# Kernel tuning notes

Measured on AMD Instinct MI355X. Metric: run time of the kernel, lower is better.

## Reference

```python
import jax, jax.numpy as jnp
import numpy as np

# config (matches init_kwargs)
B, N, C_IN = 2, 16384, 64
NPOINT, NSAMPLE, RADIUS = 2048, 32, 0.8
MLP = [64, 128, 256]
EPS = 1e-5


def _fps(xyz, npoint):
    """Furthest point sampling. xyz: (B,N,3) -> idx (B,npoint) int32."""
    b, n, _ = xyz.shape
    d0 = jnp.sum((xyz - xyz[:, :1, :]) ** 2, -1)  # dist to point 0

    def body(mind, _):
        nxt = jnp.argmax(mind, -1)                       # (B,)
        pt = jnp.take_along_axis(xyz, nxt[:, None, None], 1)  # (B,1,3)
        mind = jnp.minimum(mind, jnp.sum((xyz - pt) ** 2, -1))
        return mind, nxt

    _, idxs = jax.lax.scan(body, d0, None, length=npoint - 1)  # (npoint-1,B)
    idxs = jnp.concatenate([jnp.zeros((1, b), idxs.dtype), idxs], 0)
    return jnp.transpose(idxs).astype(jnp.int32)


def _ball_query(xyz, new_xyz, radius, nsample):
    """First nsample neighbors within radius (pointnet2 semantics: pad with first hit)."""
    n = xyz.shape[1]
    d = jnp.sum((new_xyz[:, :, None, :] - xyz[:, None, :, :]) ** 2, -1)  # (B,np,N)
    mask = d < radius * radius
    # prefer lowest original index among in-range points
    score = jnp.where(mask, -jnp.arange(n, dtype=jnp.float32), -(n + 1.0))
    vals, idxs = jax.lax.top_k(score, nsample)           # (B,np,ns)
    valid = vals > -(n + 0.5)
    idx = jnp.where(valid, idxs, idxs[..., :1])
    cnt = mask.sum(-1)                                    # (B,np)
    return idx.astype(jnp.int32), cnt


def _gather(arr, idx):  # arr (B,N,...), idx (B,...) -> (B,...,...)
    return jax.vmap(lambda a, i: a[i])(arr, idx)


def _bn_eval4(x, g, b):  # (B,C,P,S), eval-mode BN with running mean 0 / var 1
    s = g / jnp.sqrt(1.0 + EPS)
    return x * s[None, :, None, None] + b[None, :, None, None]


def _bn_eval3(x, g, b):  # (B,C,S)
    s = g / jnp.sqrt(1.0 + EPS)
    return x * s[None, :, None] + b[None, :, None]


def setup_inputs() -> dict:
    key = jax.random.key(0)
    ks = jax.random.split(key, 12)
    xyz = jax.random.normal(ks[0], (B, N, 3), jnp.float32)
    features = jax.random.normal(ks[1], (B, C_IN, N), jnp.float32)
    cin = 3 + C_IN
    dims = [cin] + MLP
    inp = {"xyz": xyz, "features": features}
    for li in range(3):
        w = jax.random.normal(ks[2 + li], (dims[li + 1], dims[li]), jnp.float32) / np.sqrt(dims[li])
        inp[f"W{li+1}"] = w
        inp[f"g{li+1}"] = jnp.ones((dims[li + 1],), jnp.float32)
        inp[f"b{li+1}"] = jnp.zeros((dims[li + 1],), jnp.float32)
    npt8, cd, cd8 = NPOINT // 8, MLP[-1], MLP[-1] // 8
    inp["Wq"] = jax.random.normal(ks[5], (npt8, NPOINT), jnp.float32) / np.sqrt(NPOINT)
    inp["gq"] = jnp.ones((npt8,), jnp.float32)
    inp["bq"] = jnp.zeros((npt8,), jnp.float32)
    inp["Wk"] = jax.random.normal(ks[6], (npt8, NPOINT), jnp.float32) / np.sqrt(NPOINT)
    inp["gk"] = jnp.ones((npt8,), jnp.float32)
    inp["bk"] = jnp.zeros((npt8,), jnp.float32)
    inp["We1"] = jax.random.normal(ks[7], (cd8, cd), jnp.float32) / np.sqrt(cd)
    inp["We2"] = jax.random.normal(ks[8], (cd, cd8), jnp.float32) / np.sqrt(cd8)
    inp["alpha"] = jnp.zeros((1,), jnp.float32)  # torch: nn.Parameter(torch.zeros(1))
    return inp


def reference(xyz, features, W1, g1, b1, W2, g2, b2, W3, g3, b3,
              Wq, gq, bq, Wk, gk, bk, We1, We2, alpha):
    # ---- d-FPS sampling (indices are non-differentiable, as in the CUDA op) ----
    xyz_c = jax.lax.stop_gradient(xyz)
    samp = _fps(xyz_c, NPOINT)                       # (B,np)
    new_xyz = _gather(xyz, samp)                     # (B,np,3)
    # ---- ball query + grouping ----
    nn_idx, cnt = _ball_query(xyz_c, jax.lax.stop_gradient(new_xyz), RADIUS, NSAMPLE)
    grouped_xyz = _gather(xyz, nn_idx) - new_xyz[:, :, None, :]        # (B,np,ns,3)
    grouped_feat = _gather(jnp.transpose(features, (0, 2, 1)), nn_idx)  # (B,np,ns,C)
    h = jnp.transpose(jnp.concatenate([grouped_xyz, grouped_feat], -1), (0, 3, 1, 2))  # (B,3+C,np,ns)
    # ---- shared MLP (1x1 conv + BN(eval) + ReLU) ----
    for (w, g, b) in ((W1, g1, b1), (W2, g2, b2), (W3, g3, b3)):
        h = jax.nn.relu(_bn_eval4(jnp.einsum('oi,bips->bops', w, h), g, b))
    h = h * (cnt > 0)[:, None, :, None].astype(h.dtype)  # mask empty balls
    x = jnp.max(h, axis=-1)                               # (B,Cd,np) max-pool over nsample
    # ---- LCEF channel-affinity attention ----
    xh = jnp.transpose(x, (0, 2, 1))                      # (B,np,Cd)
    q = jax.nn.relu(_bn_eval3(jnp.einsum('oi,bis->bos', Wq, xh), gq, bq))  # (B,np/8,Cd)
    k = jax.nn.relu(_bn_eval3(jnp.einsum('oi,bis->bos', Wk, xh), gk, bk))  # (B,np/8,Cd)
    sim = jnp.einsum('bqc,bqd->bcd', k, q)                # (B,Cd,Cd)
    aff = jax.nn.softmax(jnp.max(sim, -1, keepdims=True) - sim, axis=-1)
    s = jnp.max(x, -1)                                    # (B,Cd) squeeze
    e = jax.nn.sigmoid(jnp.einsum('oi,bi->bo', We2, jax.nn.relu(jnp.einsum('oi,bi->bo', We1, s))))
    v = x * e[:, :, None]                                 # excitation
    out = alpha[0] * jnp.einsum('bcd,bdn->bcn', aff, v) + x
    return new_xyz, out
```

## Files before the change

kernel.cpp:

```cpp
#include <hip/hip_runtime.h>
#include <hip/hip_bf16.h>

typedef unsigned short ushort_t;
typedef unsigned int uint_t;
typedef unsigned long long ull_t;
typedef float v2f __attribute__((ext_vector_type(2)));

#define B_    2
#define N_    16384
#define NP_   2048
#define NS_   32
#define EPSF  1e-5f

__device__ __forceinline__ float bf2f(ushort_t u) { return __uint_as_float(((uint_t)u) << 16); }

__device__ __forceinline__ float dist2(float dx, float dy, float dz) {
  return __fadd_rn(__fadd_rn(__fmul_rn(dx, dx), __fmul_rn(dy, dy)), __fmul_rn(dz, dz));
}

template<int CTRL, int RMASK>
__device__ __forceinline__ float dppmax(float x) {
  int m = __builtin_amdgcn_update_dpp(0, __float_as_int(x), CTRL, RMASK, 0xf, true);
  return fmaxf(x, __int_as_float(m));
}
__device__ __forceinline__ float rlanef(float x, int l) {
  return __int_as_float(__builtin_amdgcn_readlane(__float_as_int(x), l));
}

__global__ void k_flag(const uint_t* __restrict__ g1w, int* __restrict__ flag) {
  if (threadIdx.x == 0 && blockIdx.x == 0)
    flag[0] = (g1w[0] == 0x3F803F80u) ? 1 : 0;
}

struct CvtTab { const void* src[18]; };
__constant__ int c_psz[18] = {4288, 64, 64, 8192, 128, 128, 32768, 256, 256,
                              524288, 256, 256, 524288, 256, 256, 8192, 8192, 1};
__constant__ int c_poff[18] = {0, 4288, 4352, 4416, 12608, 12736, 12864, 45632, 45888,
                               46144, 570432, 570688, 570944, 1095232, 1095488,
                               1095744, 1103936, 1112128};

__global__ void k_cvt_all(CvtTab tab, float* __restrict__ par, const int* __restrict__ flagp) {
  int p = blockIdx.y;
  int n = c_psz[p];
  int i = blockIdx.x * 256 + threadIdx.x;
  if (i >= n) return;
  float v = flagp[0] ? bf2f(((const ushort_t*)tab.src[p])[i]) : ((const float*)tab.src[p])[i];
  par[c_poff[p] + i] = v;
}

__global__ void k_wt(const float* __restrict__ W1f, const float* __restrict__ W2f,
                     const float* __restrict__ W3f, float* __restrict__ Wt) {
  int which = blockIdx.y;
  int i = blockIdx.x * 256 + threadIdx.x;
  if (which == 0) {
    if (i >= 4288) return;
    int o = i / 67, k = i - o * 67;
    Wt[k * 64 + o] = W1f[i];
  } else if (which == 1) {
    if (i >= 8192) return;
    int o = i >> 6, k = i & 63;
    Wt[4288 + k * 128 + o] = W2f[i];
  } else {
    if (i >= 32768) return;
    int o = i >> 7, k = i & 127;
    Wt[12480 + k * 256 + o] = W3f[i];
  }
}

__global__ void k_xyz_soa(const void* __restrict__ xyz, const int* __restrict__ flagp,
                          float* __restrict__ X, float* __restrict__ Y, float* __restrict__ Z) {
  int g = blockIdx.x * blockDim.x + threadIdx.x;
  if (g >= B_ * N_) return;
  if (flagp[0]) {
    const ushort_t* p = (const ushort_t*)xyz;
    X[g] = bf2f(p[g * 3 + 0]); Y[g] = bf2f(p[g * 3 + 1]); Z[g] = bf2f(p[g * 3 + 2]);
  } else {
    const float* p = (const float*)xyz;
    X[g] = p[g * 3 + 0]; Y[g] = p[g * 3 + 1]; Z[g] = p[g * 3 + 2];
  }
}

__global__ void k_featT(const void* __restrict__ feat, const int* __restrict__ flagp,
                        float* __restrict__ featF) {
  __shared__ float tile[64 * 65];
  int b = blockIdx.x >> 8, n0 = (blockIdx.x & 255) * 64, t = threadIdx.x;
  int f = flagp[0];
  for (int i = t; i < 4096; i += 256) {
    int c = i >> 6, nn = i & 63;
    size_t src = (size_t)(b * 64 + c) * N_ + n0 + nn;
    tile[c * 65 + nn] = f ? bf2f(((const ushort_t*)feat)[src]) : ((const float*)feat)[src];
  }
  __syncthreads();
  for (int i = t; i < 4096; i += 256) {
    int nn = i >> 6, c = i & 63;
    featF[((size_t)(b * N_ + n0 + nn)) * 64 + c] = tile[c * 65 + nn];
  }
}

__global__ __launch_bounds__(1024)
__attribute__((amdgpu_waves_per_eu(4, 4)))
void k_fps13(const float* __restrict__ X,
             const float* __restrict__ Y,
             const float* __restrict__ Z,
             float* __restrict__ nxf,
             void* __restrict__ outp,
             const int* __restrict__ flagp) {
  __shared__ float sv[16];
  __shared__ float bc[4];
  int b = blockIdx.x, t = threadIdx.x;
  int lane = t & 63, wid = t >> 6;
  int f = flagp[0];
  const float* Xb = X + b * N_;
  const float* Yb = Y + b * N_;
  const float* Zb = Z + b * N_;
  float cx = Xb[0], cy = Yb[0], cz = Zb[0];
  if (t == 0) {
    int base = b * NP_ * 3;
    nxf[base + 0] = cx; nxf[base + 1] = cy; nxf[base + 2] = cz;
    if (f) {
      __hip_bfloat16* o = (__hip_bfloat16*)outp;
      o[base + 0] = __float2bfloat16(cx); o[base + 1] = __float2bfloat16(cy); o[base + 2] = __float2bfloat16(cz);
    } else {
      float* o = (float*)outp;
      o[base + 0] = cx; o[base + 1] = cy; o[base + 2] = cz;
    }
  }
  v2f xv[8], yv[8], zv[8], mdv[8];
  {
#pragma clang fp contract(off)
    v2f cx2 = (v2f){cx, cx}, cy2 = (v2f){cy, cy}, cz2 = (v2f){cz, cz};
#pragma unroll
    for (int c = 0; c < 4; c++) {
      float4 xq = ((const float4*)Xb)[(t << 2) + c];
      float4 yq = ((const float4*)Yb)[(t << 2) + c];
      float4 zq = ((const float4*)Zb)[(t << 2) + c];
      xv[2 * c + 0] = (v2f){xq.x, xq.y}; xv[2 * c + 1] = (v2f){xq.z, xq.w};
      yv[2 * c + 0] = (v2f){yq.x, yq.y}; yv[2 * c + 1] = (v2f){yq.z, yq.w};
      zv[2 * c + 0] = (v2f){zq.x, zq.y}; zv[2 * c + 1] = (v2f){zq.z, zq.w};
#pragma unroll
      for (int h = 0; h < 2; h++) {
        int i = 2 * c + h;
        v2f dx = xv[i] - cx2;
        v2f dy = yv[i] - cy2;
        v2f dz = zv[i] - cz2;
        mdv[i] = dx * dx + dy * dy + dz * dz;
      }
    }
  }
#pragma unroll
  for (int k = 0; k < 8; k++)
    asm volatile("" : "+v"(xv[k]), "+v"(yv[k]), "+v"(zv[k]));

  for (int it = 1; it < NP_; it++) {
    float a0 = fmaxf(fmaxf(mdv[0].x, mdv[0].y), fmaxf(mdv[1].x, mdv[1].y));
    float a1 = fmaxf(fmaxf(mdv[2].x, mdv[2].y), fmaxf(mdv[3].x, mdv[3].y));
    float a2 = fmaxf(fmaxf(mdv[4].x, mdv[4].y), fmaxf(mdv[5].x, mdv[5].y));
    float a3 = fmaxf(fmaxf(mdv[6].x, mdv[6].y), fmaxf(mdv[7].x, mdv[7].y));
    float lm = fmaxf(fmaxf(a0, a1), fmaxf(a2, a3));
    float v = lm;
    v = dppmax<0x111, 0xf>(v);
    v = dppmax<0x112, 0xf>(v);
    v = dppmax<0x114, 0xf>(v);
    v = dppmax<0x118, 0xf>(v);
    v = dppmax<0x142, 0xa>(v);
    v = dppmax<0x143, 0xc>(v);
    float wm = rlanef(v, 63);
    ull_t m1 = __ballot(lm == wm);
    int wlead = __ffsll((unsigned long long)m1) - 1;
    if (lane == wlead) sv[wid] = wm;
    __syncthreads();
    float pv = sv[lane & 15];
    float q = pv;
    q = dppmax<0x111, 0xf>(q);
    q = dppmax<0x112, 0xf>(q);
    q = dppmax<0x114, 0xf>(q);
    q = dppmax<0x118, 0xf>(q);
    float bm = rlanef(q, 15);
    ull_t m2 = __ballot((lane < 16) && (pv == bm));
    int wwave = __ffsll((unsigned long long)m2) - 1;
    if (wid == wwave && lane == wlead) {
      float wx = xv[0].x, wy = yv[0].x, wz = zv[0].x;
#pragma unroll
      for (int k = 15; k >= 0; k--) {
        float mk = (k & 1) ? mdv[k >> 1].y : mdv[k >> 1].x;
        if (mk == lm) {
          wx = (k & 1) ? xv[k >> 1].y : xv[k >> 1].x;
          wy = (k & 1) ? yv[k >> 1].y : yv[k >> 1].x;
          wz = (k & 1) ? zv[k >> 1].y : zv[k >> 1].x;
        }
      }
      bc[0] = wx; bc[1] = wy; bc[2] = wz;
      int base = (b * NP_ + it) * 3;
      nxf[base + 0] = wx; nxf[base + 1] = wy; nxf[base + 2] = wz;
      if (f) {
        __hip_bfloat16* o = (__hip_bfloat16*)outp;
        o[base + 0] = __float2bfloat16(wx); o[base + 1] = __float2bfloat16(wy); o[base + 2] = __float2bfloat16(wz);
      } else {
        float* o = (float*)outp;
        o[base + 0] = wx; o[base + 1] = wy; o[base + 2] = wz;
      }
    }
    __syncthreads();
    cx = bc[0]; cy = bc[1]; cz = bc[2];
    {
#pragma clang fp contract(off)
      v2f cx2 = (v2f){cx, cx}, cy2 = (v2f){cy, cy}, cz2 = (v2f){cz, cz};
#pragma unroll
      for (int k = 0; k < 8; k++) {
        v2f dx = xv[k] - cx2;
        v2f dy = yv[k] - cy2;
        v2f dz = zv[k] - cz2;
        v2f d = dx * dx + dy * dy + dz * dz;
        mdv[k] = __builtin_elementwise_min(mdv[k], d);
      }
    }
  }
}

__global__ void k_ball(const float* __restrict__ X, const float* __restrict__ Y,
                       const float* __restrict__ Z, const float* __restrict__ nxf,
                       int* __restrict__ nnidx) {
  __shared__ int ibuf[4][NS_];
  int t = threadIdx.x, w = t >> 6, lane = t & 63;
  int cid = blockIdx.x * 4 + w;
  int b = cid >> 11;
  const float* Xb = X + b * N_;
  const float* Yb = Y + b * N_;
  const float* Zb = Z + b * N_;
  float cx = nxf[cid * 3 + 0], cy = nxf[cid * 3 + 1], cz = nxf[cid * 3 + 2];
  int found = 0;
  for (int c = 0; c < N_ / 64; c++) {
    int n = c * 64 + lane;
    float d = dist2(Xb[n] - cx, Yb[n] - cy, Zb[n] - cz);
    bool pred = d < 0.64f;
    ull_t mask = __ballot(pred);
    if (pred) {
      int rank = found + __popcll(mask & ((1ull << lane) - 1ull));
      if (rank < NS_) ibuf[w][rank] = n;
    }
    found += __popcll(mask);
    if (found >= NS_) break;
  }
  __syncthreads();
  if (lane < NS_) {
    int idx = (lane < found) ? ibuf[w][lane] : ibuf[w][0];
    nnidx[cid * NS_ + lane] = idx;
  }
}

__global__ __launch_bounds__(256) void k_mlp(
    const float* __restrict__ featF, const float* __restrict__ X,
    const float* __restrict__ Y, const float* __restrict__ Z,
    const float* __restrict__ nxf, const int* __restrict__ nnidx,
    const float* __restrict__ Wt,
    const float* __restrict__ g1f, const float* __restrict__ b1f,
    const float* __restrict__ g2f, const float* __restrict__ b2f,
    const float* __restrict__ g3f, const float* __restrict__ b3f,
    float* __restrict__ x_nc) {
  __shared__ __align__(16) char smem[33280];
  float* h2f = (float*)smem;
  float* h0f = (float*)(smem + 16384);
  float* h1f = (float*)(smem + 24960);
  int* idxs  = (int*)(smem + 33152);
  const float* Wt1 = Wt;
  const float* Wt2 = Wt + 4288;
  const float* Wt3 = Wt + 12480;

  int t = threadIdx.x;
  int cid = blockIdx.x;
  int b = cid >> 11;
  if (t < 32) idxs[t] = nnidx[cid * NS_ + t];
  __syncthreads();
  float cx = nxf[cid * 3 + 0], cy = nxf[cid * 3 + 1], cz = nxf[cid * 3 + 2];
  if (t < 32) {
    int n = b * N_ + idxs[t];
    h0f[0 * 32 + t] = X[n] - cx;
    h0f[1 * 32 + t] = Y[n] - cy;
    h0f[2 * 32 + t] = Z[n] - cz;
  }
  {
    int s = t >> 3, cg = t & 7;
    const float* fr = featF + ((size_t)(b * N_ + idxs[s])) * 64 + cg * 8;
    float4 a = ((const float4*)fr)[0];
    float4 c2 = ((const float4*)fr)[1];
    int kb = 3 + cg * 8;
    h0f[(kb + 0) * 32 + s] = a.x;  h0f[(kb + 1) * 32 + s] = a.y;
    h0f[(kb + 2) * 32 + s] = a.z;  h0f[(kb + 3) * 32 + s] = a.w;
    h0f[(kb + 4) * 32 + s] = c2.x; h0f[(kb + 5) * 32 + s] = c2.y;
    h0f[(kb + 6) * 32 + s] = c2.z; h0f[(kb + 7) * 32 + s] = c2.w;
  }
  __syncthreads();

  int og = t >> 3, sg = t & 7;
  int s0 = sg * 4;
  {
    int o0 = og * 2;
    float acc[2][4] = {{0, 0, 0, 0}, {0, 0, 0, 0}};
    for (int k = 0; k < 67; k++) {
      float4 h = *(const float4*)(h0f + k * 32 + s0);
      float2 wp = *(const float2*)(Wt1 + k * 64 + o0);
      acc[0][0] = fmaf(wp.x, h.x, acc[0][0]);
      acc[0][1] = fmaf(wp.x, h.y, acc[0][1]);
      acc[0][2] = fmaf(wp.x, h.z, acc[0][2]);
      acc[0][3] = fmaf(wp.x, h.w, acc[0][3]);
      acc[1][0] = fmaf(wp.y, h.x, acc[1][0]);
      acc[1][1] = fmaf(wp.y, h.y, acc[1][1]);
      acc[1][2] = fmaf(wp.y, h.z, acc[1][2]);
      acc[1][3] = fmaf(wp.y, h.w, acc[1][3]);
    }
#pragma unroll
    for (int i2 = 0; i2 < 2; i2++) {
      int o = o0 + i2;
      float sc = g1f[o] / sqrtf(1.0f + EPSF);
      float bb = b1f[o];
      float4 yv;
      yv.x = fmaxf(fmaf(acc[i2][0], sc, bb), 0.0f);
      yv.y = fmaxf(fmaf(acc[i2][1], sc, bb), 0.0f);
      yv.z = fmaxf(fmaf(acc[i2][2], sc, bb), 0.0f);
      yv.w = fmaxf(fmaf(acc[i2][3], sc, bb), 0.0f);
      *(float4*)(h1f + o * 32 + s0) = yv;
    }
  }
  __syncthreads();
  {
    int o0 = og * 4;
    float acc[4][4] = {{0,0,0,0},{0,0,0,0},{0,0,0,0},{0,0,0,0}};
    for (int k = 0; k < 64; k++) {
      float4 h = *(const float4*)(h1f + k * 32 + s0);
      float4 wp = *(const float4*)(Wt2 + k * 128 + o0);
      float w[4] = {wp.x, wp.y, wp.z, wp.w};
#pragma unroll
      for (int i2 = 0; i2 < 4; i2++) {
        acc[i2][0] = fmaf(w[i2], h.x, acc[i2][0]);
        acc[i2][1] = fmaf(w[i2], h.y, acc[i2][1]);
        acc[i2][2] = fmaf(w[i2], h.z, acc[i2][2]);
        acc[i2][3] = fmaf(w[i2], h.w, acc[i2][3]);
      }
    }
#pragma unroll
    for (int i2 = 0; i2 < 4; i2++) {
      int o = o0 + i2;
      float sc = g2f[o] / sqrtf(1.0f + EPSF);
      float bb = b2f[o];
      float4 yv;
      yv.x = fmaxf(fmaf(acc[i2][0], sc, bb), 0.0f);
      yv.y = fmaxf(fmaf(acc[i2][1], sc, bb), 0.0f);
      yv.z = fmaxf(fmaf(acc[i2][2], sc, bb), 0.0f);
      yv.w = fmaxf(fmaf(acc[i2][3], sc, bb), 0.0f);
      *(float4*)(h2f + o * 32 + s0) = yv;
    }
  }
  __syncthreads();
  float acc3[8][4] = {{0,0,0,0},{0,0,0,0},{0,0,0,0},{0,0,0,0},
                      {0,0,0,0},{0,0,0,0},{0,0,0,0},{0,0,0,0}};
  int o0 = og * 8;
  for (int kg = 0; kg < 128; kg++) {
    float4 h = *(const float4*)(h2f + kg * 32 + s0);
    float4 wa = *(const float4*)(Wt3 + kg * 256 + o0);
    float4 wc = *(const float4*)(Wt3 + kg * 256 + o0 + 4);
    float w[8] = {wa.x, wa.y, wa.z, wa.w, wc.x, wc.y, wc.z, wc.w};
#pragma unroll
    for (int i2 = 0; i2 < 8; i2++) {
      acc3[i2][0] = fmaf(w[i2], h.x, acc3[i2][0]);
      acc3[i2][1] = fmaf(w[i2], h.y, acc3[i2][1]);
      acc3[i2][2] = fmaf(w[i2], h.z, acc3[i2][2]);
      acc3[i2][3] = fmaf(w[i2], h.w, acc3[i2][3]);
    }
  }
  float mx[8];
#pragma unroll
  for (int i2 = 0; i2 < 8; i2++) {
    int o = o0 + i2;
    float sc = g3f[o] / sqrtf(1.0f + EPSF);
    float bb = b3f[o];
    float m0 = fmaxf(fmaf(acc3[i2][0], sc, bb), 0.0f);
    float m1 = fmaxf(fmaf(acc3[i2][1], sc, bb), 0.0f);
    float m2 = fmaxf(fmaf(acc3[i2][2], sc, bb), 0.0f);
    float m3 = fmaxf(fmaf(acc3[i2][3], sc, bb), 0.0f);
    mx[i2] = fmaxf(fmaxf(m0, m1), fmaxf(m2, m3));
  }
#pragma unroll
  for (int off = 1; off < 8; off <<= 1) {
#pragma unroll
    for (int i2 = 0; i2 < 8; i2++) mx[i2] = fmaxf(mx[i2], __shfl_xor(mx[i2], off));
  }
  if (sg == 0) {
    float4 a, c;
    a.x = mx[0]; a.y = mx[1]; a.z = mx[2]; a.w = mx[3];
    c.x = mx[4]; c.y = mx[5]; c.z = mx[6]; c.w = mx[7];
    *(float4*)(x_nc + (size_t)cid * 256 + o0) = a;
    *(float4*)(x_nc + (size_t)cid * 256 + o0 + 4) = c;
  }
}

__global__ __launch_bounds__(256) void k_sqe(const float* __restrict__ x_nc,
                                             const float* __restrict__ We1f,
                                             const float* __restrict__ We2f,
                                             float* __restrict__ e) {
  __shared__ float ssh[256];
  __shared__ float ush[32];
  int b = blockIdx.x, t = threadIdx.x;
  const float* xb = x_nc + (size_t)b * NP_ * 256;
  float m = -1e30f;
#pragma unroll 8
  for (int n = 0; n < NP_; n++) m = fmaxf(m, xb[(size_t)n * 256 + t]);
  ssh[t] = m;
  __syncthreads();
  if (t < 32) {
    float a = 0.0f;
    for (int i = 0; i < 256; i++) a = fmaf(We1f[t * 256 + i], ssh[i], a);
    ush[t] = fmaxf(a, 0.0f);
  }
  __syncthreads();
  float a = 0.0f;
#pragma unroll
  for (int j = 0; j < 32; j++) a = fmaf(We2f[t * 32 + j], ush[j], a);
  e[b * 256 + t] = 1.0f / (1.0f + expf(-a));
}

__global__ __launch_bounds__(256) void k_qk(const float* __restrict__ x_nc,
                                            const float* __restrict__ Wqf, const float* __restrict__ gqf, const float* __restrict__ bqf,
                                            const float* __restrict__ Wkf, const float* __restrict__ gkf, const float* __restrict__ bkf,
                                            float* __restrict__ qb, float* __restrict__ kb) {
  __shared__ float As[64 * 33];
  __shared__ float Bs[32 * 64];
  int bid = blockIdx.x;
  int b = bid & 1, tq = (bid >> 1) & 1, mt = (bid >> 2) & 3, nt = (bid >> 4) & 3;
  const float* W = tq ? Wkf : Wqf;
  const float* g = tq ? gkf : gqf;
  const float* bb_ = tq ? bkf : bqf;
  float* outp = tq ? kb : qb;
  int t = threadIdx.x;
  int o0 = (t >> 4) * 4, c0 = (t & 15) * 4;
  float acc[4][4] = {{0,0,0,0},{0,0,0,0},{0,0,0,0},{0,0,0,0}};
  for (int k0 = 0; k0 < NP_; k0 += 32) {
    for (int i = t; i < 2048; i += 256) {
      int row = i >> 5, kk = i & 31;
      As[row * 33 + kk] = W[(size_t)(mt * 64 + row) * NP_ + k0 + kk];
    }
    for (int i = t; i < 2048; i += 256) {
      int kk = i >> 6, cc = i & 63;
      Bs[kk * 64 + cc] = x_nc[((size_t)(b * NP_ + k0 + kk)) * 256 + nt * 64 + cc];
    }
    __syncthreads();
    for (int kk = 0; kk < 32; kk++) {
      float4 bv = *(const float4*)(Bs + kk * 64 + c0);
      float a0 = As[(o0 + 0) * 33 + kk];
      float a1 = As[(o0 + 1) * 33 + kk];
      float a2 = As[(o0 + 2) * 33 + kk];
      float a3 = As[(o0 + 3) * 33 + kk];
      acc[0][0] = fmaf(a0, bv.x, acc[0][0]); acc[0][1] = fmaf(a0, bv.y, acc[0][1]);
      acc[0][2] = fmaf(a0, bv.z, acc[0][2]); acc[0][3] = fmaf(a0, bv.w, acc[0][3]);
      acc[1][0] = fmaf(a1, bv.x, acc[1][0]); acc[1][1] = fmaf(a1, bv.y, acc[1][1]);
      acc[1][2] = fmaf(a1, bv.z, acc[1][2]); acc[1][3] = fmaf(a1, bv.w, acc[1][3]);
      acc[2][0] = fmaf(a2, bv.x, acc[2][0]); acc[2][1] = fmaf(a2, bv.y, acc[2][1]);
      acc[2][2] = fmaf(a2, bv.z, acc[2][2]); acc[2][3] = fmaf(a2, bv.w, acc[2][3]);
      acc[3][0] = fmaf(a3, bv.x, acc[3][0]); acc[3][1] = fmaf(a3, bv.y, acc[3][1]);
      acc[3][2] = fmaf(a3, bv.z, acc[3][2]); acc[3][3] = fmaf(a3, bv.w, acc[3][3]);
    }
    __syncthreads();
  }
#pragma unroll
  for (int i2 = 0; i2 < 4; i2++) {
    int o = mt * 64 + o0 + i2;
    float sc = g[o] / sqrtf(1.0f + EPSF);
    float bv = bb_[o];
    float4 y;
    y.x = fmaxf(fmaf(acc[i2][0], sc, bv), 0.0f);
    y.y = fmaxf(fmaf(acc[i2][1], sc, bv), 0.0f);
    y.z = fmaxf(fmaf(acc[i2][2], sc, bv), 0.0f);
    y.w = fmaxf(fmaf(acc[i2][3], sc, bv), 0.0f);
    *(float4*)(outp + ((size_t)(b * 256 + o)) * 256 + nt * 64 + c0) = y;
  }
}

__global__ __launch_bounds__(256) void k_sim(const float* __restrict__ qb,
                                             const float* __restrict__ kb,
                                             float* __restrict__ sim) {
  __shared__ float As[32 * 64];
  __shared__ float Bs[32 * 64];
  int bid = blockIdx.x;
  int b = bid & 1, ct = (bid >> 1) & 3, dt = (bid >> 3) & 3;
  int t = threadIdx.x;
  int c0 = (t >> 4) * 4, d0 = (t & 15) * 4;
  float acc[4][4] = {{0,0,0,0},{0,0,0,0},{0,0,0,0},{0,0,0,0}};
  for (int k0 = 0; k0 < 256; k0 += 32) {
    for (int i = t; i < 2048; i += 256) {
      int kk = i >> 6, cc = i & 63;
      As[kk * 64 + cc] = kb[((size_t)(b * 256 + k0 + kk)) * 256 + ct * 64 + cc];
      Bs[kk * 64 + cc] = qb[((size_t)(b * 256 + k0 + kk)) * 256 + dt * 64 + cc];
    }
    __syncthreads();
    for (int kk = 0; kk < 32; kk++) {
      float4 av = *(const float4*)(As + kk * 64 + c0);
      float4 bv = *(const float4*)(Bs + kk * 64 + d0);
      acc[0][0] = fmaf(av.x, bv.x, acc[0][0]); acc[0][1] = fmaf(av.x, bv.y, acc[0][1]);
      acc[0][2] = fmaf(av.x, bv.z, acc[0][2]); acc[0][3] = fmaf(av.x, bv.w, acc[0][3]);
      acc[1][0] = fmaf(av.y, bv.x, acc[1][0]); acc[1][1] = fmaf(av.y, bv.y, acc[1][1]);
      acc[1][2] = fmaf(av.y, bv.z, acc[1][2]); acc[1][3] = fmaf(av.y, bv.w, acc[1][3]);
      acc[2][0] = fmaf(av.z, bv.x, acc[2][0]); acc[2][1] = fmaf(av.z, bv.y, acc[2][1]);
      acc[2][2] = fmaf(av.z, bv.z, acc[2][2]); acc[2][3] = fmaf(av.z, bv.w, acc[2][3]);
      acc[3][0] = fmaf(av.w, bv.x, acc[3][0]); acc[3][1] = fmaf(av.w, bv.y, acc[3][1]);
      acc[3][2] = fmaf(av.w, bv.z, acc[3][2]); acc[3][3] = fmaf(av.w, bv.w, acc[3][3]);
    }
    __syncthreads();
  }
#pragma unroll
  for (int i2 = 0; i2 < 4; i2++) {
    *(float4*)(sim + ((size_t)(b * 256 + ct * 64 + c0 + i2)) * 256 + dt * 64 + d0) =
        *(float4*)acc[i2];
  }
}

__global__ void k_aff(const float* __restrict__ sim, float* __restrict__ aff) {
  int t = threadIdx.x, w = t >> 6, lane = t & 63;
  int row = blockIdx.x * 4 + w;
  const float* sr = sim + (size_t)row * 256;
  float4 v = *(const float4*)(sr + lane * 4);
  float mx = fmaxf(fmaxf(v.x, v.y), fmaxf(v.z, v.w));
#pragma unroll
  for (int off = 32; off >= 1; off >>= 1) mx = fmaxf(mx, __shfl_xor(mx, off));
  float4 u;
  u.x = mx - v.x; u.y = mx - v.y; u.z = mx - v.z; u.w = mx - v.w;
  float um = fmaxf(fmaxf(u.x, u.y), fmaxf(u.z, u.w));
#pragma unroll
  for (int off = 32; off >= 1; off >>= 1) um = fmaxf(um, __shfl_xor(um, off));
  float4 p;
  p.x = expf(u.x - um); p.y = expf(u.y - um); p.z = expf(u.z - um); p.w = expf(u.w - um);
  float s = ((p.x + p.y) + (p.z + p.w));
#pragma unroll
  for (int off = 32; off >= 1; off >>= 1) s += __shfl_xor(s, off);
  float4 o;
  o.x = p.x / s; o.y = p.y / s; o.z = p.z / s; o.w = p.w / s;
  *(float4*)(aff + (size_t)row * 256 + lane * 4) = o;
}

__global__ __launch_bounds__(256) void k_out(const float* __restrict__ aff,
                                             const float* __restrict__ x_nc,
                                             const float* __restrict__ e,
                                             const float* __restrict__ alphaf,
                                             void* __restrict__ outp,
                                             const int* __restrict__ flagp) {
  __shared__ float Acs[64 * 33];
  __shared__ float Bs[32 * 65];
  __shared__ float Xs[64 * 65];
  int bid = blockIdx.x;
  int b = bid & 1, ct = (bid >> 1) & 3, nt = bid >> 3;
  int t = threadIdx.x;
  int c0 = (t >> 4) * 4, n0 = (t & 15) * 4;
  float acc[4][4] = {{0,0,0,0},{0,0,0,0},{0,0,0,0},{0,0,0,0}};
  for (int k0 = 0; k0 < 256; k0 += 32) {
    for (int i = t; i < 2048; i += 256) {
      int cc = i >> 5, kk = i & 31;
      Acs[cc * 33 + kk] = aff[((size_t)(b * 256 + ct * 64 + cc)) * 256 + k0 + kk];
    }
    for (int i = t; i < 2048; i += 256) {
      int nn = i >> 5, kk = i & 31;
      Bs[kk * 65 + nn] =
          x_nc[((size_t)(b * NP_ + nt * 64 + nn)) * 256 + k0 + kk] * e[b * 256 + k0 + kk];
    }
    __syncthreads();
    for (int kk = 0; kk < 32; kk++) {
      float a0 = Acs[(c0 + 0) * 33 + kk];
      float a1 = Acs[(c0 + 1) * 33 + kk];
      float a2 = Acs[(c0 + 2) * 33 + kk];
      float a3 = Acs[(c0 + 3) * 33 + kk];
      float b0 = Bs[kk * 65 + n0 + 0];
      float b1 = Bs[kk * 65 + n0 + 1];
      float b2 = Bs[kk * 65 + n0 + 2];
      float b3 = Bs[kk * 65 + n0 + 3];
      acc[0][0] = fmaf(a0, b0, acc[0][0]); acc[0][1] = fmaf(a0, b1, acc[0][1]);
      acc[0][2] = fmaf(a0, b2, acc[0][2]); acc[0][3] = fmaf(a0, b3, acc[0][3]);
      acc[1][0] = fmaf(a1, b0, acc[1][0]); acc[1][1] = fmaf(a1, b1, acc[1][1]);
      acc[1][2] = fmaf(a1, b2, acc[1][2]); acc[1][3] = fmaf(a1, b3, acc[1][3]);
      acc[2][0] = fmaf(a2, b0, acc[2][0]); acc[2][1] = fmaf(a2, b1, acc[2][1]);
      acc[2][2] = fmaf(a2, b2, acc[2][2]); acc[2][3] = fmaf(a2, b3, acc[2][3]);
      acc[3][0] = fmaf(a3, b0, acc[3][0]); acc[3][1] = fmaf(a3, b1, acc[3][1]);
      acc[3][2] = fmaf(a3, b2, acc[3][2]); acc[3][3] = fmaf(a3, b3, acc[3][3]);
    }
    __syncthreads();
  }
  for (int i = t; i < 4096; i += 256) {
    int nn = i >> 6, cc = i & 63;
    Xs[nn * 65 + cc] = x_nc[((size_t)(b * NP_ + nt * 64 + nn)) * 256 + ct * 64 + cc];
  }
  __syncthreads();
  float af = alphaf[0];
  int f = flagp[0];
#pragma unroll
  for (int i2 = 0; i2 < 4; i2++) {
    int c = ct * 64 + c0 + i2;
#pragma unroll
    for (int j = 0; j < 4; j++) {
      float xv = Xs[(n0 + j) * 65 + (c0 + i2)];
      float y = af * acc[i2][j] + xv;
      size_t base = 12288 + ((size_t)(b * 256 + c)) * NP_ + nt * 64 + n0 + j;
      if (f) ((__hip_bfloat16*)outp)[base] = __float2bfloat16(y);
      else   ((float*)outp)[base] = y;
    }
  }
}

extern "C" void kernel_launch(void* const* d_in, const int* in_sizes, int n_in,
                              void* d_out, int out_size, void* d_ws, size_t ws_size,
                              hipStream_t stream) {
  char* ws = (char*)d_ws;
  int*   flag  = (int*)(ws + 0);
  float* X     = (float*)(ws + 64);
  float* Y     = (float*)(ws + 131136);
  float* Z     = (float*)(ws + 262208);
  float* featF = (float*)(ws + 393280);
  float* par   = (float*)(ws + 8781888);
  float* nxf   = (float*)(ws + 13230464);
  int*   nn    = (int*)(ws + 13279616);
  float* x_nc  = (float*)(ws + 13803904);
  float* qb    = (float*)(ws + 17998208);
  float* kb    = (float*)(ws + 18522496);
  float* sim   = (float*)(ws + 19046784);
  float* aff   = (float*)(ws + 19571072);
  float* evec  = (float*)(ws + 20095360);
  float* Wt    = qb;

  float* W1f = par + 0,      *g1f = par + 4288,    *b1f = par + 4352;
  float* W2f = par + 4416,   *g2f = par + 12608,   *b2f = par + 12736;
  float* W3f = par + 12864,  *g3f = par + 45632,   *b3f = par + 45888;
  float* Wqf = par + 46144,  *gqf = par + 570432,  *bqf = par + 570688;
  float* Wkf = par + 570944, *gkf = par + 1095232, *bkf = par + 1095488;
  float* We1f = par + 1095744, *We2f = par + 1103936, *alphaf = par + 1112128;

  k_flag<<<dim3(1), dim3(64), 0, stream>>>((const uint_t*)d_in[3], flag);

  CvtTab tab;
  for (int p = 0; p < 18; p++) tab.src[p] = d_in[2 + p];
  k_cvt_all<<<dim3(2048, 18), dim3(256), 0, stream>>>(tab, par, flag);
  k_wt<<<dim3(128, 3), dim3(256), 0, stream>>>(W1f, W2f, W3f, Wt);

  k_xyz_soa<<<dim3(128), dim3(256), 0, stream>>>(d_in[0], flag, X, Y, Z);
  k_featT<<<dim3(512), dim3(256), 0, stream>>>(d_in[1], flag, featF);
  k_fps13<<<dim3(2), dim3(1024), 0, stream>>>(X, Y, Z, nxf, d_out, flag);
  k_ball<<<dim3(1024), dim3(256), 0, stream>>>(X, Y, Z, nxf, nn);
  k_mlp<<<dim3(4096), dim3(256), 0, stream>>>(featF, X, Y, Z, nxf, nn, Wt,
                                              g1f, b1f, g2f, b2f, g3f, b3f, x_nc);
  k_sqe<<<dim3(2), dim3(256), 0, stream>>>(x_nc, We1f, We2f, evec);
  k_qk<<<dim3(64), dim3(256), 0, stream>>>(x_nc, Wqf, gqf, bqf, Wkf, gkf, bkf, qb, kb);
  k_sim<<<dim3(32), dim3(256), 0, stream>>>(qb, kb, sim);
  k_aff<<<dim3(128), dim3(256), 0, stream>>>(sim, aff);
  k_out<<<dim3(256), dim3(256), 0, stream>>>(aff, x_nc, evec, alphaf, d_out, flag);
}
```

Baseline: 4.094 ms.

## Remove second per-iteration barrier in FPS via double-buffered per-wave candidates

Each wave leader now finds its own candidate point coordinates and writes value plus xyz into a double-buffered shared array. After the single barrier, every thread picks the winning wave's coordinates directly, so the second __syncthreads and the broadcast slot are gone. The local max reduction also uses packed v2f max operations. Every wave leader now does the 16-way coordinate selection, adding a little redundant work and shared memory to halve the barrier count per iteration.

```diff
diff --git a/kernel.cpp b/kernel.cpp
--- a/kernel.cpp
+++ b/kernel.cpp
@@ -99,14 +99,16 @@
 
 __global__ __launch_bounds__(1024)
 __attribute__((amdgpu_waves_per_eu(4, 4)))
-void k_fps13(const float* __restrict__ X,
+void k_fps14(const float* __restrict__ X,
              const float* __restrict__ Y,
              const float* __restrict__ Z,
              float* __restrict__ nxf,
              void* __restrict__ outp,
              const int* __restrict__ flagp) {
-  __shared__ float sv[16];
-  __shared__ float bc[4];
+  __shared__ float sv[2][16];
+  __shared__ float sx[2][16];
+  __shared__ float sy[2][16];
+  __shared__ float sz[2][16];
   int b = blockIdx.x, t = threadIdx.x;
   int lane = t & 63, wid = t >> 6;
   int f = flagp[0];
@@ -152,11 +154,15 @@
     asm volatile("" : "+v"(xv[k]), "+v"(yv[k]), "+v"(zv[k]));
 
   for (int it = 1; it < NP_; it++) {
-    float a0 = fmaxf(fmaxf(mdv[0].x, mdv[0].y), fmaxf(mdv[1].x, mdv[1].y));
-    float a1 = fmaxf(fmaxf(mdv[2].x, mdv[2].y), fmaxf(mdv[3].x, mdv[3].y));
-    float a2 = fmaxf(fmaxf(mdv[4].x, mdv[4].y), fmaxf(mdv[5].x, mdv[5].y));
-    float a3 = fmaxf(fmaxf(mdv[6].x, mdv[6].y), fmaxf(mdv[7].x, mdv[7].y));
-    float lm = fmaxf(fmaxf(a0, a1), fmaxf(a2, a3));
+    int buf = it & 1;
+    v2f m01 = __builtin_elementwise_max(mdv[0], mdv[1]);
+    v2f m23 = __builtin_elementwise_max(mdv[2], mdv[3]);
+    v2f m45 = __builtin_elementwise_max(mdv[4], mdv[5]);
+    v2f m67 = __builtin_elementwise_max(mdv[6], mdv[7]);
+    v2f m03 = __builtin_elementwise_max(m01, m23);
+    v2f m47 = __builtin_elementwise_max(m45, m67);
+    v2f m07 = __builtin_elementwise_max(m03, m47);
+    float lm = fmaxf(m07.x, m07.y);
     float v = lm;
     v = dppmax<0x111, 0xf>(v);
     v = dppmax<0x112, 0xf>(v);
@@ -167,9 +173,24 @@
     float wm = rlanef(v, 63);
     ull_t m1 = __ballot(lm == wm);
     int wlead = __ffsll((unsigned long long)m1) - 1;
-    if (lane == wlead) sv[wid] = wm;
+    if (lane == wlead) {
+      float wx = xv[0].x, wy = yv[0].x, wz = zv[0].x;
+#pragma unroll
+      for (int k = 15; k >= 0; k--) {
+        float mk = (k & 1) ? mdv[k >> 1].y : mdv[k >> 1].x;
+        if (mk == lm) {
+          wx = (k & 1) ? xv[k >> 1].y : xv[k >> 1].x;
+          wy = (k & 1) ? yv[k >> 1].y : yv[k >> 1].x;
+          wz = (k & 1) ? zv[k >> 1].y : zv[k >> 1].x;
+        }
+      }
+      sv[buf][wid] = lm;
+      sx[buf][wid] = wx;
+      sy[buf][wid] = wy;
+      sz[buf][wid] = wz;
+    }
     __syncthreads();
-    float pv = sv[lane & 15];
+    float pv = sv[buf][lane & 15];
     float q = pv;
     q = dppmax<0x111, 0xf>(q);
     q = dppmax<0x112, 0xf>(q);
@@ -178,30 +199,20 @@
     float bm = rlanef(q, 15);
     ull_t m2 = __ballot((lane < 16) && (pv == bm));
     int wwave = __ffsll((unsigned long long)m2) - 1;
-    if (wid == wwave && lane == wlead) {
-      float wx = xv[0].x, wy = yv[0].x, wz = zv[0].x;
-#pragma unroll
-      for (int k = 15; k >= 0; k--) {
-        float mk = (k & 1) ? mdv[k >> 1].y : mdv[k >> 1].x;
-        if (mk == lm) {
-          wx = (k & 1) ? xv[k >> 1].y : xv[k >> 1].x;
-          wy = (k & 1) ? yv[k >> 1].y : yv[k >> 1].x;
-          wz = (k & 1) ? zv[k >> 1].y : zv[k >> 1].x;
-        }
-      }
-      bc[0] = wx; bc[1] = wy; bc[2] = wz;
+    cx = sx[buf][wwave];
+    cy = sy[buf][wwave];
+    cz = sz[buf][wwave];
+    if (t == 0) {
       int base = (b * NP_ + it) * 3;
-      nxf[base + 0] = wx; nxf[base + 1] = wy; nxf[base + 2] = wz;
+      nxf[base + 0] = cx; nxf[base + 1] = cy; nxf[base + 2] = cz;
       if (f) {
         __hip_bfloat16* o = (__hip_bfloat16*)outp;
-        o[base + 0] = __float2bfloat16(wx); o[base + 1] = __float2bfloat16(wy); o[base + 2] = __float2bfloat16(wz);
+        o[base + 0] = __float2bfloat16(cx); o[base + 1] = __float2bfloat16(cy); o[base + 2] = __float2bfloat16(cz);
       } else {
         float* o = (float*)outp;
-        o[base + 0] = wx; o[base + 1] = wy; o[base + 2] = wz;
+        o[base + 0] = cx; o[base + 1] = cy; o[base + 2] = cz;
       }
     }
-    __syncthreads();
-    cx = bc[0]; cy = bc[1]; cz = bc[2];
     {
 #pragma clang fp contract(off)
       v2f cx2 = (v2f){cx, cx}, cy2 = (v2f){cy, cy}, cz2 = (v2f){cz, cz};
@@ -637,7 +648,7 @@
 
   k_xyz_soa<<<dim3(128), dim3(256), 0, stream>>>(d_in[0], flag, X, Y, Z);
   k_featT<<<dim3(512), dim3(256), 0, stream>>>(d_in[1], flag, featF);
-  k_fps13<<<dim3(2), dim3(1024), 0, stream>>>(X, Y, Z, nxf, d_out, flag);
+  k_fps14<<<dim3(2), dim3(1024), 0, stream>>>(X, Y, Z, nxf, d_out, flag);
   k_ball<<<dim3(1024), dim3(256), 0, stream>>>(X, Y, Z, nxf, nn);
   k_mlp<<<dim3(4096), dim3(256), 0, stream>>>(featF, X, Y, Z, nxf, nn, Wt,
                                               g1f, b1f, g2f, b2f, g3f, b3f, x_nc);
```

New measurement: 5.300 ms. 29.5% more time.
